# Optimization experiments

Measured on AMD Instinct MI355X. Metric: run time of the kernel, lower is better.

## Reference

```python
import jax, jax.numpy as jnp
import numpy as np

L, B, D, H, FFN, V = 6, 16, 1024, 16, 4096, 32000
CACHE, SRC, MAXPOS = 512, 512, 1024
HD = D // H
SCALING = HD ** -0.5


def _sinusoidal_pe():
    # MarianMT format: first half sin, second half cos (not interleaved)
    half = D // 2
    emb = np.exp(np.arange(half, dtype=np.float32) * (-np.log(10000.0) / (half - 1)))
    pos = np.arange(MAXPOS, dtype=np.float32)[:, None]
    pe = np.concatenate([np.sin(pos * emb), np.cos(pos * emb)], axis=1)
    return jnp.asarray(pe, jnp.float32)


def setup_inputs() -> dict:
    key = jax.random.key(0)
    keys = iter(jax.random.split(key, 64))
    def rn(shape, s=0.02):
        return jax.random.normal(next(keys), shape, jnp.float32) * s
    inp = {
        'decoder_embed': rn((B, 1, D), 1.0),
        'encoder_hidden_states': rn((B, SRC, D), 1.0),
        'past_keys': rn((L, B, CACHE, D), 1.0),
        'past_values': rn((L, B, CACHE, D), 1.0),
        'cache_len': jnp.array([256], jnp.int32),
        'pe': _sinusoidal_pe(),
    }
    for name in ['sa_qw', 'sa_kw', 'sa_vw', 'sa_ow', 'ca_qw', 'ca_kw', 'ca_vw', 'ca_ow']:
        inp[name] = rn((L, D, D))
    for name in ['sa_qb', 'sa_kb', 'sa_vb', 'sa_ob', 'ca_qb', 'ca_kb', 'ca_vb', 'ca_ob']:
        inp[name] = rn((L, D))
    inp['fc1_w'] = rn((L, FFN, D)); inp['fc1_b'] = rn((L, FFN))
    inp['fc2_w'] = rn((L, D, FFN)); inp['fc2_b'] = rn((L, D))
    for name in ['ln1_w', 'ln2_w', 'ln3_w']:
        inp[name] = jnp.ones((L, D), jnp.float32)
    for name in ['ln1_b', 'ln2_b', 'ln3_b']:
        inp[name] = jnp.zeros((L, D), jnp.float32)
    inp['lm_w'] = rn((V, D))
    return inp


def _lin(x, w, b):
    # torch nn.Linear: w is [out, in]
    return jnp.einsum('...i,oi->...o', x, w) + b


def _ln(x, w, b):
    m = jnp.mean(x, -1, keepdims=True)
    v = jnp.var(x, -1, keepdims=True)
    return (x - m) * jax.lax.rsqrt(v + 1e-5) * w + b


def _heads(x):
    # [B, S, D] -> [B, H, S, HD]
    b, s, _ = x.shape
    return x.reshape(b, s, H, HD).transpose(0, 2, 1, 3)


def _attend(q, k, v, bias):
    w = jnp.einsum('bhqd,bhkd->bhqk', q * SCALING, k)
    if bias is not None:
        w = w + bias
    a = jax.nn.softmax(w, axis=-1)
    o = jnp.einsum('bhqk,bhkd->bhqd', a, v)
    b = o.shape[0]
    return o.transpose(0, 2, 1, 3).reshape(b, -1, D)


def reference(decoder_embed, encoder_hidden_states, past_keys, past_values, cache_len, pe,
              sa_qw, sa_kw, sa_vw, sa_ow, ca_qw, ca_kw, ca_vw, ca_ow,
              sa_qb, sa_kb, sa_vb, sa_ob, ca_qb, ca_kb, ca_vb, ca_ob,
              fc1_w, fc1_b, fc2_w, fc2_b,
              ln1_w, ln1_b, ln2_w, ln2_b, ln3_w, ln3_b, lm_w):
    embed_scale = jnp.asarray(np.sqrt(float(D)), jnp.float32)
    pos = jax.lax.dynamic_slice_in_dim(pe, cache_len[0], 1, axis=0)[None]  # [1,1,D]
    h = decoder_embed * embed_scale + pos
    # Faithful to original: cache_len tensor is passed as attn_mask and
    # broadcast-added to attention logits (a constant shift, no-op post-softmax).
    mask_bias = cache_len.astype(h.dtype)
    new_ks, new_vs = [], []
    for i in range(L):
        # self-attention with KV cache concat
        res = h
        q = _lin(h, sa_qw[i], sa_qb[i])
        nk = _lin(h, sa_kw[i], sa_kb[i])
        nv = _lin(h, sa_vw[i], sa_vb[i])
        fk = jnp.concatenate([past_keys[i], nk], axis=1)   # [B, CACHE+1, D]
        fv = jnp.concatenate([past_values[i], nv], axis=1)
        attn = _attend(_heads(q), _heads(fk), _heads(fv), mask_bias)
        h = _ln(res + _lin(attn, sa_ow[i], sa_ob[i]), ln1_w[i], ln1_b[i])
        # cross-attention (no mask)
        res = h
        q = _lin(h, ca_qw[i], ca_qb[i])
        ek = _lin(encoder_hidden_states, ca_kw[i], ca_kb[i])
        ev = _lin(encoder_hidden_states, ca_vw[i], ca_vb[i])
        attn = _attend(_heads(q), _heads(ek), _heads(ev), None)
        h = _ln(res + _lin(attn, ca_ow[i], ca_ob[i]), ln2_w[i], ln2_b[i])
        # FFN with SiLU
        res = h
        ff = _lin(jax.nn.silu(_lin(h, fc1_w[i], fc1_b[i])), fc2_w[i], fc2_b[i])
        h = _ln(res + ff, ln3_w[i], ln3_b[i])
        new_ks.append(nk)
        new_vs.append(nv)
    logits = jnp.einsum('bsd,vd->bsv', h, lm_w)  # lm_head, no bias
    return (logits, jnp.stack(new_ks, 0), jnp.stack(new_vs, 0))
```

## Files before the change

kernel.cpp:

```cpp
#include <hip/hip_runtime.h>
#include <math.h>

#define LYRS 6
#define BATCH 16
#define DIM 1024
#define NH 16
#define HDIM 64
#define FFNDIM 4096
#define VOCAB 32000
#define NCACHE 512
#define SRCLEN 512
#define SCALE 0.125f
#define EMB_SCALE 32.0f
#define BD (BATCH * DIM)
#define BF (BATCH * FFNDIM)
#define BV (BATCH * VOCAB)

__device__ __forceinline__ float wave_reduce_sum(float v){
#pragma unroll
  for (int off = 32; off; off >>= 1) v += __shfl_xor(v, off, 64);
  return v;
}
__device__ __forceinline__ float wave_reduce_max(float v){
#pragma unroll
  for (int off = 32; off; off >>= 1) v = fmaxf(v, __shfl_xor(v, off, 64));
  return v;
}
__device__ __forceinline__ float4 silu4(float4 v){
  v.x = v.x / (1.f + __expf(-v.x));
  v.y = v.y / (1.f + __expf(-v.y));
  v.z = v.z / (1.f + __expf(-v.z));
  v.w = v.w / (1.f + __expf(-v.w));
  return v;
}

__global__ __launch_bounds__(256) void k_embed(const float* __restrict__ de,
                                               const float* __restrict__ pe,
                                               const int* __restrict__ cl,
                                               float* __restrict__ h){
  int b = blockIdx.x, t = threadIdx.x;
  int c = cl[0];
  const float4* d4 = (const float4*)(de + (size_t)b * DIM);
  const float4* p4 = (const float4*)(pe + (size_t)c * DIM);
  float4* h4 = (float4*)(h + (size_t)b * DIM);
  float4 a = d4[t], p = p4[t];
  float4 o;
  o.x = a.x * EMB_SCALE + p.x; o.y = a.y * EMB_SCALE + p.y;
  o.z = a.z * EMB_SCALE + p.z; o.w = a.w * EMB_SCALE + p.w;
  h4[t] = o;
}

template<int KPB, int NZ, bool SILU>
__device__ __forceinline__ void gemv_ms_core(
    const float* __restrict__ Asrc, int a_rs, int pz,
    const float* __restrict__ abias,
    const float* __restrict__ W, int w_rs,
    float* __restrict__ Cz, int c_rs,
    int n0, int k0){
  __shared__ float As[16][KPB];
  const int tid = threadIdx.x;
  {
    const int m = tid >> 4;
    const int q0 = (tid & 15) * 4;
    constexpr int QPT = KPB / 64;
#pragma unroll
    for (int qq = 0; qq < QPT; ++qq){
      const int q = q0 + qq * 64;
      const int gk = k0 + q;
      float4 v;
      if (NZ == 0){
        v = *(const float4*)(Asrc + (size_t)m * a_rs + gk);
      } else {
        if (abias) v = *(const float4*)(abias + gk);
        else { v.x = 0.f; v.y = 0.f; v.z = 0.f; v.w = 0.f; }
#pragma unroll
        for (int z = 0; z < NZ; ++z){
          float4 pv = *(const float4*)(Asrc + (size_t)z * pz + (size_t)m * a_rs + gk);
          v.x += pv.x; v.y += pv.y; v.z += pv.z; v.w += pv.w;
        }
      }
      if (SILU) v = silu4(v);
      *(float4*)(&As[m][q]) = v;
    }
  }
  __syncthreads();
  const int lane = tid & 63;
  const int m0 = (tid >> 6) * 4;
  const float* Wrow = W + (size_t)(n0 + lane) * w_rs + k0;
  float acc0 = 0.f, acc1 = 0.f, acc2 = 0.f, acc3 = 0.f;
  constexpr int CHUNKS = KPB / 64;
  float4 wb[2][16];
#pragma unroll
  for (int c = 0; c < 16; ++c) wb[0][c] = *(const float4*)(Wrow + c * 4);
#pragma unroll
  for (int ch = 0; ch < CHUNKS; ++ch){
    const int cur = ch & 1;
    if (ch + 1 < CHUNKS){
#pragma unroll
      for (int c = 0; c < 16; ++c)
        wb[cur ^ 1][c] = *(const float4*)(Wrow + (ch + 1) * 64 + c * 4);
    }
#pragma unroll
    for (int c = 0; c < 16; ++c){
      float4 wv = wb[cur][c];
      const int q = ch * 64 + c * 4;
      float4 a0 = *(const float4*)(&As[m0 + 0][q]);
      float4 a1 = *(const float4*)(&As[m0 + 1][q]);
      float4 a2 = *(const float4*)(&As[m0 + 2][q]);
      float4 a3 = *(const float4*)(&As[m0 + 3][q]);
      acc0 = fmaf(wv.x, a0.x, acc0); acc0 = fmaf(wv.y, a0.y, acc0);
      acc0 = fmaf(wv.z, a0.z, acc0); acc0 = fmaf(wv.w, a0.w, acc0);
      acc1 = fmaf(wv.x, a1.x, acc1); acc1 = fmaf(wv.y, a1.y, acc1);
      acc1 = fmaf(wv.z, a1.z, acc1); acc1 = fmaf(wv.w, a1.w, acc1);
      acc2 = fmaf(wv.x, a2.x, acc2); acc2 = fmaf(wv.y, a2.y, acc2);
      acc2 = fmaf(wv.z, a2.z, acc2); acc2 = fmaf(wv.w, a2.w, acc2);
      acc3 = fmaf(wv.x, a3.x, acc3); acc3 = fmaf(wv.y, a3.y, acc3);
      acc3 = fmaf(wv.z, a3.z, acc3); acc3 = fmaf(wv.w, a3.w, acc3);
    }
  }
  Cz[(size_t)(m0 + 0) * c_rs + n0 + lane] = acc0;
  Cz[(size_t)(m0 + 1) * c_rs + n0 + lane] = acc1;
  Cz[(size_t)(m0 + 2) * c_rs + n0 + lane] = acc2;
  Cz[(size_t)(m0 + 3) * c_rs + n0 + lane] = acc3;
}

template<int KPB, int NZ, bool SILU>
__global__ __launch_bounds__(256) void k_gemv_ms(
    const float* __restrict__ A, int a_rs, int a_bs, int pz,
    const float* __restrict__ abias,
    const float* __restrict__ W, int w_rs, int w_bs,
    float* __restrict__ C, int c_rs, int c_bs, int c_zs){
  const int bb = blockIdx.y;
  gemv_ms_core<KPB, NZ, SILU>(A + (size_t)bb * a_bs, a_rs, pz, abias,
      W + (size_t)bb * w_bs, w_rs,
      C + (size_t)blockIdx.z * c_zs + (size_t)bb * c_bs, c_rs,
      blockIdx.x * 64, blockIdx.z * KPB);
}

template<int KPB>
__global__ __launch_bounds__(256) void k_gemv_ms3(
    const float* __restrict__ A, const float* __restrict__ W0,
    const float* __restrict__ W1, const float* __restrict__ W2,
    float* __restrict__ C){
  const int y = blockIdx.y;
  const float* W = (y == 0) ? W0 : ((y == 1) ? W1 : W2);
  gemv_ms_core<KPB, 0, false>(A, DIM, 0, nullptr, W, DIM,
      C + ((size_t)y * 4 + blockIdx.z) * BD, DIM,
      blockIdx.x * 64, blockIdx.z * KPB);
}

__global__ __launch_bounds__(256) void k_fin2(const float* __restrict__ P,
                                              float* __restrict__ out){
  int i = blockIdx.x * 256 + threadIdx.x;
  out[i] = P[i] + P[(size_t)BV + i];
}

__global__ __launch_bounds__(512) void k_self_attn(
    const float* __restrict__ Pqkv, const float* __restrict__ qb_,
    const float* __restrict__ kb_, const float* __restrict__ vb_,
    const float* __restrict__ pk, const float* __restrict__ pv,
    float* __restrict__ satt, float* __restrict__ out_k,
    float* __restrict__ out_v){
  __shared__ float qs[64], ks[64], vs[64];
  __shared__ float sc[513];
  __shared__ float red1[8], red2[8];
  __shared__ float o8[8][64];
  const int bh = blockIdx.x, b = bh >> 4, h = bh & 15;
  const int tid = threadIdx.x, w = tid >> 6, lane = tid & 63;
  const int hd = h * HDIM + lane;
  if (w < 3){
    const float* Pz = Pqkv + (size_t)w * (4 * BD);
    const float* bias = (w == 0) ? qb_ : ((w == 1) ? kb_ : vb_);
    float v = bias[hd];
#pragma unroll
    for (int z = 0; z < 4; ++z)
      v += Pz[(size_t)z * BD + b * DIM + hd];
    if (w == 0) qs[lane] = v * SCALE;
    else if (w == 1){ ks[lane] = v; out_k[b * DIM + hd] = v; }
    else { vs[lane] = v; out_v[b * DIM + hd] = v; }
  }
  __syncthreads();
  const int jj = lane >> 4, c = lane & 15;
  float4 q4 = *(const float4*)(&qs[c * 4]);
  const float* kbase = pk + (size_t)b * NCACHE * DIM + h * HDIM + c * 4;
  {
    float4 nk = *(const float4*)(kbase + (size_t)(w * 4 + jj) * DIM);
    for (int it = 0; it < 16; ++it){
      int j = it * 32 + w * 4 + jj;
      float4 K4 = nk;
      if (it < 15) nk = *(const float4*)(kbase + (size_t)(j + 32) * DIM);
      float r = q4.x * K4.x;
      r = fmaf(q4.y, K4.y, r); r = fmaf(q4.z, K4.z, r); r = fmaf(q4.w, K4.w, r);
      r += __shfl_xor(r, 1, 64); r += __shfl_xor(r, 2, 64);
      r += __shfl_xor(r, 4, 64); r += __shfl_xor(r, 8, 64);
      if (c == 0) sc[j] = r;
    }
  }
  if (w == 0 && lane < 16){
    float4 k4 = *(const float4*)(&ks[lane * 4]);
    float r = q4.x * k4.x;
    r = fmaf(q4.y, k4.y, r); r = fmaf(q4.z, k4.z, r); r = fmaf(q4.w, k4.w, r);
    r += __shfl_xor(r, 1, 64); r += __shfl_xor(r, 2, 64);
// ... 26 lines not shown
  float4 acc; acc.x = 0.f; acc.y = 0.f; acc.z = 0.f; acc.w = 0.f;
  {
    float4 nv = *(const float4*)(vbase + (size_t)(w * 4 + jj) * DIM);
    for (int it = 0; it < 16; ++it){
      int j = it * 32 + w * 4 + jj;
      float4 V4 = nv;
      if (it < 15) nv = *(const float4*)(vbase + (size_t)(j + 32) * DIM);
      float pj = sc[j];
      acc.x = fmaf(pj, V4.x, acc.x); acc.y = fmaf(pj, V4.y, acc.y);
      acc.z = fmaf(pj, V4.z, acc.z); acc.w = fmaf(pj, V4.w, acc.w);
    }
  }
  if (w == 0 && lane < 16){
    float p512 = sc[512];
    float4 v4 = *(const float4*)(&vs[lane * 4]);
    acc.x = fmaf(p512, v4.x, acc.x); acc.y = fmaf(p512, v4.y, acc.y);
    acc.z = fmaf(p512, v4.z, acc.z); acc.w = fmaf(p512, v4.w, acc.w);
  }
  acc.x += __shfl_xor(acc.x, 16, 64); acc.x += __shfl_xor(acc.x, 32, 64);
  acc.y += __shfl_xor(acc.y, 16, 64); acc.y += __shfl_xor(acc.y, 32, 64);
  acc.z += __shfl_xor(acc.z, 16, 64); acc.z += __shfl_xor(acc.z, 32, 64);
  acc.w += __shfl_xor(acc.w, 16, 64); acc.w += __shfl_xor(acc.w, 32, 64);
  if (lane < 16){
    o8[w][lane * 4 + 0] = acc.x; o8[w][lane * 4 + 1] = acc.y;
    o8[w][lane * 4 + 2] = acc.z; o8[w][lane * 4 + 3] = acc.w;
  }
  __syncthreads();
  if (tid < 64){
    float s2 = 0.f;
#pragma unroll
    for (int ww = 0; ww < 8; ++ww) s2 += o8[ww][tid];
    satt[b * DIM + h * HDIM + tid] = s2 * inv;
  }
}

template<int NZ>
__global__ __launch_bounds__(256) void k_add_ln_pz(
    const float* __restrict__ res, const float* __restrict__ P, int zs,
    const float* __restrict__ obias, const float* __restrict__ w,
    const float* __restrict__ bln, float* __restrict__ outh){
  __shared__ float r1[4], r2[4];
  int b = blockIdx.x, tid = threadIdx.x, wave = tid >> 6, lane = tid & 63;
  float4 rv = ((const float4*)(res + (size_t)b * DIM))[tid];
  float4 ob = ((const float4*)obias)[tid];
  float v0 = rv.x + ob.x, v1 = rv.y + ob.y, v2 = rv.z + ob.z, v3 = rv.w + ob.w;
#pragma unroll
  for (int z = 0; z < NZ; ++z){
    float4 pz = ((const float4*)(P + (size_t)z * zs + (size_t)b * DIM))[tid];
    v0 += pz.x; v1 += pz.y; v2 += pz.z; v3 += pz.w;
  }
  float s = v0 + v1 + v2 + v3;
  float sq = v0 * v0 + v1 * v1 + v2 * v2 + v3 * v3;
  s = wave_reduce_sum(s); sq = wave_reduce_sum(sq);
  if (lane == 0){ r1[wave] = s; r2[wave] = sq; }
  __syncthreads();
  float ts = r1[0] + r1[1] + r1[2] + r1[3];
  float tq = r2[0] + r2[1] + r2[2] + r2[3];
  float mean = ts * (1.f / DIM);
  float var = tq * (1.f / DIM) - mean * mean;
  float rstd = rsqrtf(var + 1e-5f);
  float4 wv = ((const float4*)w)[tid], bv = ((const float4*)bln)[tid];
  float4 o;
  o.x = (v0 - mean) * rstd * wv.x + bv.x;
  o.y = (v1 - mean) * rstd * wv.y + bv.y;
  o.z = (v2 - mean) * rstd * wv.z + bv.z;
  o.w = (v3 - mean) * rstd * wv.w + bv.w;
  ((float4*)(outh + (size_t)b * DIM))[tid] = o;
}

__global__ __launch_bounds__(256) void k_gmat2(
    const float* __restrict__ Pcq, const float* __restrict__ caqb,
    const float* __restrict__ kw, float* __restrict__ g){
  __shared__ float qsT[64][16];
  __shared__ float Ps[4][16][64];
  const int h = blockIdx.y, c0 = blockIdx.x * 64;
  const int tid = threadIdx.x, lane = tid & 63, wave = tid >> 6;
  {
    const int b = tid >> 4, q0 = (tid & 15) * 4;
    float4 v = *(const float4*)(caqb + h * HDIM + q0);
#pragma unroll
    for (int z = 0; z < 8; ++z){
      float4 pv = *(const float4*)(Pcq + (size_t)z * BD +
                                   (size_t)b * DIM + h * HDIM + q0);
      v.x += pv.x; v.y += pv.y; v.z += pv.z; v.w += pv.w;
    }
    qsT[q0 + 0][b] = v.x * SCALE; qsT[q0 + 1][b] = v.y * SCALE;
    qsT[q0 + 2][b] = v.z * SCALE; qsT[q0 + 3][b] = v.w * SCALE;
  }
  __syncthreads();
  float wv[16];
#pragma unroll
  for (int dd = 0; dd < 16; ++dd)
    wv[dd] = kw[(size_t)(h * HDIM + wave * 16 + dd) * DIM + c0 + lane];
  float acc[16];
#pragma unroll
  for (int m = 0; m < 16; ++m) acc[m] = 0.f;
#pragma unroll
  for (int dd = 0; dd < 16; ++dd){
    const int d = wave * 16 + dd;
    float4 a0 = *(const float4*)(&qsT[d][0]);
// ... 119 lines not shown
  const float* pv   = (const float*)d_in[3];
  const int*   cl   = (const int*)d_in[4];
  const float* pe   = (const float*)d_in[5];
  const float* saqw = (const float*)d_in[6];
  const float* sakw = (const float*)d_in[7];
  const float* savw = (const float*)d_in[8];
  const float* saow = (const float*)d_in[9];
  const float* caqw = (const float*)d_in[10];
  const float* cakw = (const float*)d_in[11];
  const float* cavw = (const float*)d_in[12];
  const float* caow = (const float*)d_in[13];
  const float* saqb = (const float*)d_in[14];
  const float* sakb = (const float*)d_in[15];
  const float* savb = (const float*)d_in[16];
  const float* saob = (const float*)d_in[17];
  const float* caqb = (const float*)d_in[18];
  const float* cakb = (const float*)d_in[19];
  const float* cavb = (const float*)d_in[20];
  const float* caob = (const float*)d_in[21];
  const float* fc1w = (const float*)d_in[22];
  const float* fc1b = (const float*)d_in[23];
  const float* fc2w = (const float*)d_in[24];
  const float* fc2b = (const float*)d_in[25];
  const float* ln1w = (const float*)d_in[26];
  const float* ln2w = (const float*)d_in[27];
  const float* ln3w = (const float*)d_in[28];
  const float* ln1b = (const float*)d_in[29];
  const float* ln2b = (const float*)d_in[30];
  const float* ln3b = (const float*)d_in[31];
  const float* lmw  = (const float*)d_in[32];
  float* out = (float*)d_out;
  float* ws  = (float*)d_ws;

  float* h    = ws;
  float* satt = ws + 16384;
  float* g    = ws + 32768;
  float* ctx  = ws + 294912;
  float* Pqkv = ws + 557056;
  float* Po   = ws + 950272;
  float* Pcq  = ws + 1212416;
  float* Pvo  = ws + 1474560;
  float* Pco  = ws + 1736704;
  float* Pf1  = ws + 1998848;
  float* Pf2  = ws + 2523136;
  float* s2b  = ws + 3047424;
  float* Plm  = ws + 4096000;

  float* out_k = out + 512000;
  float* out_v = out + 610304;

  k_embed<<<16, 256, 0, stream>>>(de, pe, cl, h);

  for (int i = 0; i < LYRS; ++i){
    size_t wo = (size_t)i * DIM * DIM;
    size_t bo = (size_t)i * DIM;
    float* ko = out_k + (size_t)i * BD;
    float* vo = out_v + (size_t)i * BD;
    k_gemv_ms3<256><<<dim3(16, 3, 4), 256, 0, stream>>>(h, saqw + wo, sakw + wo,
        savw + wo, Pqkv);
    k_self_attn<<<256, 512, 0, stream>>>(Pqkv, saqb + bo, sakb + bo, savb + bo,
        pk + (size_t)i * BATCH * NCACHE * DIM, pv + (size_t)i * BATCH * NCACHE * DIM,
        satt, ko, vo);
    k_gemv_ms<128, 0, false><<<dim3(16, 1, 8), 256, 0, stream>>>(satt, DIM, 0, 0,
        nullptr, saow + wo, DIM, 0, Po, DIM, 0, BD);
    k_add_ln_pz<8><<<16, 256, 0, stream>>>(h, Po, BD, saob + bo,
        ln1w + bo, ln1b + bo, h);
    k_gemv_ms<128, 0, false><<<dim3(16, 1, 8), 256, 0, stream>>>(h, DIM, 0, 0,
        nullptr, caqw + wo, DIM, 0, Pcq, DIM, 0, BD);
    k_gmat2<<<dim3(16, 16), 256, 0, stream>>>(Pcq, caqb + bo, cakw + wo, g);
    k_gemv_ms<512, 0, false><<<dim3(8, 16, 2), 256, 0, stream>>>(g, DIM, NH * DIM,
        0, nullptr, enc, DIM, SRCLEN * DIM, s2b, SRCLEN, NH * SRCLEN,
        BATCH * NH * SRCLEN);
    k_ctx_sm<<<dim3(16, 16), 256, 0, stream>>>(s2b, enc, ctx);
    k_gemv_ms<128, 0, false><<<dim3(1, 16, 8), 256, 0, stream>>>(ctx, NH * DIM,
        DIM, 0, nullptr, cavw + wo, DIM, HDIM * DIM, Pvo, DIM, HDIM, BD);
    k_gemv_ms<128, 8, false><<<dim3(16, 1, 8), 256, 0, stream>>>(Pvo, DIM, 0,
        BD, cavb + bo, caow + wo, DIM, 0, Pco, DIM, 0, BD);
    k_add_ln_pz<8><<<16, 256, 0, stream>>>(h, Pco, BD, caob + bo,
        ln2w + bo, ln2b + bo, h);
    k_gemv_ms<256, 0, false><<<dim3(64, 1, 4), 256, 0, stream>>>(h, DIM, 0, 0,
        nullptr, fc1w + (size_t)i * FFNDIM * DIM, DIM, 0, Pf1, FFNDIM, 0, BF);
    k_gemv_ms<128, 4, true><<<dim3(16, 1, 32), 256, 0, stream>>>(Pf1, FFNDIM, 0,
        BF, fc1b + (size_t)i * FFNDIM,
        fc2w + (size_t)i * DIM * FFNDIM, FFNDIM, 0, Pf2, DIM, 0, BD);
    k_add_ln_pz<32><<<16, 256, 0, stream>>>(h, Pf2, BD, fc2b + bo,
        ln3w + bo, ln3b + bo, h);
  }
  k_gemv_ms<512, 0, false><<<dim3(VOCAB / 64, 1, 2), 256, 0, stream>>>(h, DIM, 0,
      0, nullptr, lmw, DIM, 0, Plm, VOCAB, 0, BV);
  k_fin2<<<BV / 256, 256, 0, stream>>>(Plm, out);
}
```

Baseline: 847.1 us.

## Fuse residual-add LayerNorm into following GEMV prologues and use atomic split-K

```diff
diff --git a/kernel.cpp b/kernel.cpp
--- a/kernel.cpp
+++ b/kernel.cpp
@@ -51,40 +51,85 @@
 }
 
 template<int KPB, int NZ, bool SILU>
-__device__ __forceinline__ void gemv_ms_core(
+__device__ __forceinline__ void plain_stage(float (*As)[KPB],
     const float* __restrict__ Asrc, int a_rs, int pz,
-    const float* __restrict__ abias,
-    const float* __restrict__ W, int w_rs,
-    float* __restrict__ Cz, int c_rs,
-    int n0, int k0){
-  __shared__ float As[16][KPB];
+    const float* __restrict__ abias, int k0){
   const int tid = threadIdx.x;
-  {
-    const int m = tid >> 4;
-    const int q0 = (tid & 15) * 4;
-    constexpr int QPT = KPB / 64;
-#pragma unroll
-    for (int qq = 0; qq < QPT; ++qq){
-      const int q = q0 + qq * 64;
-      const int gk = k0 + q;
-      float4 v;
-      if (NZ == 0){
-        v = *(const float4*)(Asrc + (size_t)m * a_rs + gk);
-      } else {
-        if (abias) v = *(const float4*)(abias + gk);
-        else { v.x = 0.f; v.y = 0.f; v.z = 0.f; v.w = 0.f; }
-#pragma unroll
-        for (int z = 0; z < NZ; ++z){
-          float4 pv = *(const float4*)(Asrc + (size_t)z * pz + (size_t)m * a_rs + gk);
-          v.x += pv.x; v.y += pv.y; v.z += pv.z; v.w += pv.w;
-        }
+  const int m = tid >> 4, q0 = (tid & 15) * 4;
+#pragma unroll
+  for (int qq = 0; qq < KPB / 64; ++qq){
+    const int q = q0 + qq * 64;
+    const int gk = k0 + q;
+    float4 v;
+    if (NZ == 0){
+      v = *(const float4*)(Asrc + (size_t)m * a_rs + gk);
+    } else {
+      if (abias) v = *(const float4*)(abias + gk);
+      else { v.x = 0.f; v.y = 0.f; v.z = 0.f; v.w = 0.f; }
+#pragma unroll
+      for (int z = 0; z < NZ; ++z){
+        float4 pv = *(const float4*)(Asrc + (size_t)z * pz + (size_t)m * a_rs + gk);
+        v.x += pv.x; v.y += pv.y; v.z += pv.z; v.w += pv.w;
       }
-      if (SILU) v = silu4(v);
-      *(float4*)(&As[m][q]) = v;
-    }
-  }
-  __syncthreads();
-  const int lane = tid & 63;
+    }
+    if (SILU) v = silu4(v);
+    *(float4*)(&As[m][q]) = v;
+  }
+  __syncthreads();
+}
+
+template<int KPB>
+__device__ __forceinline__ void ln_stage(float (*As)[KPB],
+    const float* __restrict__ res, const float* __restrict__ acc,
+    const float* __restrict__ obias, const float* __restrict__ lnw,
+    const float* __restrict__ lnb, int k0, float* __restrict__ hout){
+  const int tid = threadIdx.x;
+  const int m = tid >> 4, t = tid & 15;
+  const float* rr = res + (size_t)m * DIM;
+  const float* ar = acc + (size_t)m * DIM;
+  float s = 0.f, sq = 0.f;
+#pragma unroll
+  for (int c = 0; c < 16; ++c){
+    const int k = t * 4 + c * 64;
+    float4 rv = *(const float4*)(rr + k);
+    float4 av = *(const float4*)(ar + k);
+    float4 ob = *(const float4*)(obias + k);
+    float x0 = rv.x + av.x + ob.x, x1 = rv.y + av.y + ob.y;
+    float x2 = rv.z + av.z + ob.z, x3 = rv.w + av.w + ob.w;
+    s += x0 + x1 + x2 + x3;
+    sq += x0 * x0 + x1 * x1 + x2 * x2 + x3 * x3;
+  }
+#pragma unroll
+  for (int o = 1; o <= 8; o <<= 1){
+    s += __shfl_xor(s, o, 64); sq += __shfl_xor(sq, o, 64);
+  }
+  const float mean = s * (1.f / DIM);
+  const float rstd = rsqrtf(sq * (1.f / DIM) - mean * mean + 1e-5f);
+#pragma unroll
+  for (int qq = 0; qq < KPB / 64; ++qq){
+    const int q = t * 4 + qq * 64;
+    const int k = k0 + q;
+    float4 rv = *(const float4*)(rr + k);
+    float4 av = *(const float4*)(ar + k);
+    float4 ob = *(const float4*)(obias + k);
+    float4 wv = *(const float4*)(lnw + k);
+    float4 bv = *(const float4*)(lnb + k);
+    float4 o4;
+    o4.x = (rv.x + av.x + ob.x - mean) * rstd * wv.x + bv.x;
+    o4.y = (rv.y + av.y + ob.y - mean) * rstd * wv.y + bv.y;
+    o4.z = (rv.z + av.z + ob.z - mean) * rstd * wv.z + bv.z;
+    o4.w = (rv.w + av.w + ob.w - mean) * rstd * wv.w + bv.w;
+    *(float4*)(&As[m][q]) = o4;
+    if (hout) *(float4*)(hout + (size_t)m * DIM + k) = o4;
+  }
+  __syncthreads();
+}
+
+template<int KPB, bool ATOMIC>
+__device__ __forceinline__ void gemv_w_loop(float (*As)[KPB],
+    const float* __restrict__ W, int w_rs, float* __restrict__ Cz,
+    int c_rs, int n0, int k0){
+  const int tid = threadIdx.x, lane = tid & 63;
   const int m0 = (tid >> 6) * 4;
   const float* Wrow = W + (size_t)(n0 + lane) * w_rs + k0;
   float acc0 = 0.f, acc1 = 0.f, acc2 = 0.f, acc3 = 0.f;
@@ -118,21 +163,30 @@
       acc3 = fmaf(wv.z, a3.z, acc3); acc3 = fmaf(wv.w, a3.w, acc3);
     }
   }
-  Cz[(size_t)(m0 + 0) * c_rs + n0 + lane] = acc0;
-  Cz[(size_t)(m0 + 1) * c_rs + n0 + lane] = acc1;
-  Cz[(size_t)(m0 + 2) * c_rs + n0 + lane] = acc2;
-  Cz[(size_t)(m0 + 3) * c_rs + n0 + lane] = acc3;
-}
-
-template<int KPB, int NZ, bool SILU>
+  if (ATOMIC){
+    atomicAdd(&Cz[(size_t)(m0 + 0) * c_rs + n0 + lane], acc0);
+    atomicAdd(&Cz[(size_t)(m0 + 1) * c_rs + n0 + lane], acc1);
+    atomicAdd(&Cz[(size_t)(m0 + 2) * c_rs + n0 + lane], acc2);
+    atomicAdd(&Cz[(size_t)(m0 + 3) * c_rs + n0 + lane], acc3);
+  } else {
+    Cz[(size_t)(m0 + 0) * c_rs + n0 + lane] = acc0;
+    Cz[(size_t)(m0 + 1) * c_rs + n0 + lane] = acc1;
+    Cz[(size_t)(m0 + 2) * c_rs + n0 + lane] = acc2;
+    Cz[(size_t)(m0 + 3) * c_rs + n0 + lane] = acc3;
+  }
+}
+
+template<int KPB, int NZ, bool SILU, bool ATOMIC>
 __global__ __launch_bounds__(256) void k_gemv_ms(
     const float* __restrict__ A, int a_rs, int a_bs, int pz,
     const float* __restrict__ abias,
     const float* __restrict__ W, int w_rs, int w_bs,
     float* __restrict__ C, int c_rs, int c_bs, int c_zs){
+  __shared__ float As[16][KPB];
   const int bb = blockIdx.y;
-  gemv_ms_core<KPB, NZ, SILU>(A + (size_t)bb * a_bs, a_rs, pz, abias,
-      W + (size_t)bb * w_bs, w_rs,
+  plain_stage<KPB, NZ, SILU>(As, A + (size_t)bb * a_bs, a_rs, pz, abias,
+                             blockIdx.z * KPB);
+  gemv_w_loop<KPB, ATOMIC>(As, W + (size_t)bb * w_bs, w_rs,
       C + (size_t)blockIdx.z * c_zs + (size_t)bb * c_bs, c_rs,
       blockIdx.x * 64, blockIdx.z * KPB);
 }
@@ -142,9 +196,42 @@
     const float* __restrict__ A, const float* __restrict__ W0,
     const float* __restrict__ W1, const float* __restrict__ W2,
     float* __restrict__ C){
+  __shared__ float As[16][KPB];
   const int y = blockIdx.y;
   const float* W = (y == 0) ? W0 : ((y == 1) ? W1 : W2);
-  gemv_ms_core<KPB, 0, false>(A, DIM, 0, nullptr, W, DIM,
+  plain_stage<KPB, 0, false>(As, A, DIM, 0, nullptr, blockIdx.z * KPB);
+  gemv_w_loop<KPB, false>(As, W, DIM,
+      C + ((size_t)y * 4 + blockIdx.z) * BD, DIM,
+      blockIdx.x * 64, blockIdx.z * KPB);
+}
+
+template<int KPB>
+__global__ __launch_bounds__(256) void k_gemv_ln(
+    const float* __restrict__ res, const float* __restrict__ acc,
+    const float* __restrict__ obias, const float* __restrict__ lnw,
+    const float* __restrict__ lnb, const float* __restrict__ W,
+    float* __restrict__ hout, float* __restrict__ C, int c_rs, int c_zs){
+  __shared__ float As[16][KPB];
+  float* hw = (blockIdx.x == 0) ? hout : nullptr;
+  ln_stage<KPB>(As, res, acc, obias, lnw, lnb, blockIdx.z * KPB, hw);
+  gemv_w_loop<KPB, false>(As, W, DIM, C + (size_t)blockIdx.z * c_zs, c_rs,
+      blockIdx.x * 64, blockIdx.z * KPB);
+}
+
+template<int KPB>
+__global__ __launch_bounds__(256) void k_gemv_ln3(
+    const float* __restrict__ res, const float* __restrict__ acc,
+    const float* __restrict__ obias, const float* __restrict__ lnw,
+    const float* __restrict__ lnb,
+    const float* __restrict__ W0, const float* __restrict__ W1,
+    const float* __restrict__ W2,
+    float* __restrict__ hout, float* __restrict__ C){
+  __shared__ float As[16][KPB];
+  const int y = blockIdx.y;
+  const float* W = (y == 0) ? W0 : ((y == 1) ? W1 : W2);
+  float* hw = (blockIdx.x == 0 && y == 0) ? hout : nullptr;
+  ln_stage<KPB>(As, res, acc, obias, lnw, lnb, blockIdx.z * KPB, hw);
+  gemv_w_loop<KPB, false>(As, W, DIM,
       C + ((size_t)y * 4 + blockIdx.z) * BD, DIM,
       blockIdx.x * 64, blockIdx.z * KPB);
 }
@@ -160,7 +247,7 @@
     const float* __restrict__ kb_, const float* __restrict__ vb_,
     const float* __restrict__ pk, const float* __restrict__ pv,
     float* __restrict__ satt, float* __restrict__ out_k,
-    float* __restrict__ out_v){
+    float* __restrict__ out_v, float* __restrict__ azero){
   __shared__ float qs[64], ks[64], vs[64];
   __shared__ float sc[513];
   __shared__ float red1[8], red2[8];
@@ -168,6 +255,10 @@
   const int bh = blockIdx.x, b = bh >> 4, h = bh & 15;
   const int tid = threadIdx.x, w = tid >> 6, lane = tid & 63;
   const int hd = h * HDIM + lane;
+  if (tid < 48){
+    float4 z4; z4.x = 0.f; z4.y = 0.f; z4.z = 0.f; z4.w = 0.f;
+    ((float4*)azero)[(size_t)bh * 48 + tid] = z4;
+  }
   if (w < 3){
     const float* Pz = Pqkv + (size_t)w * (4 * BD);
     const float* bias = (w == 0) ? qb_ : ((w == 1) ? kb_ : vb_);
@@ -260,40 +351,6 @@
     for (int ww = 0; ww < 8; ++ww) s2 += o8[ww][tid];
     satt[b * DIM + h * HDIM + tid] = s2 * inv;
   }
-}
-
-template<int NZ>
-__global__ __launch_bounds__(256) void k_add_ln_pz(
-    const float* __restrict__ res, const float* __restrict__ P, int zs,
-    const float* __restrict__ obias, const float* __restrict__ w,
-    const float* __restrict__ bln, float* __restrict__ outh){
-  __shared__ float r1[4], r2[4];
-  int b = blockIdx.x, tid = threadIdx.x, wave = tid >> 6, lane = tid & 63;
-  float4 rv = ((const float4*)(res + (size_t)b * DIM))[tid];
-  float4 ob = ((const float4*)obias)[tid];
-  float v0 = rv.x + ob.x, v1 = rv.y + ob.y, v2 = rv.z + ob.z, v3 = rv.w + ob.w;
-#pragma unroll
-  for (int z = 0; z < NZ; ++z){
-    float4 pz = ((const float4*)(P + (size_t)z * zs + (size_t)b * DIM))[tid];
-    v0 += pz.x; v1 += pz.y; v2 += pz.z; v3 += pz.w;
-  }
-  float s = v0 + v1 + v2 + v3;
-  float sq = v0 * v0 + v1 * v1 + v2 * v2 + v3 * v3;
-  s = wave_reduce_sum(s); sq = wave_reduce_sum(sq);
-  if (lane == 0){ r1[wave] = s; r2[wave] = sq; }
-  __syncthreads();
-  float ts = r1[0] + r1[1] + r1[2] + r1[3];
-  float tq = r2[0] + r2[1] + r2[2] + r2[3];
-  float mean = ts * (1.f / DIM);
-  float var = tq * (1.f / DIM) - mean * mean;
-  float rstd = rsqrtf(var + 1e-5f);
-  float4 wv = ((const float4*)w)[tid], bv = ((const float4*)bln)[tid];
-  float4 o;
-  o.x = (v0 - mean) * rstd * wv.x + bv.x;
-  o.y = (v1 - mean) * rstd * wv.y + bv.y;
-  o.z = (v2 - mean) * rstd * wv.z + bv.z;
-  o.w = (v3 - mean) * rstd * wv.w + bv.w;
-  ((float4*)(outh + (size_t)b * DIM))[tid] = o;
 }
 
 __global__ __launch_bounds__(256) void k_gmat2(
@@ -479,61 +536,70 @@
   float* out = (float*)d_out;
   float* ws  = (float*)d_ws;
 
-  float* h    = ws;
-  float* satt = ws + 16384;
-  float* g    = ws + 32768;
-  float* ctx  = ws + 294912;
-  float* Pqkv = ws + 557056;
-  float* Po   = ws + 950272;
-  float* Pcq  = ws + 1212416;
-  float* Pvo  = ws + 1474560;
-  float* Pco  = ws + 1736704;
-  float* Pf1  = ws + 1998848;
-  float* Pf2  = ws + 2523136;
-  float* s2b  = ws + 3047424;
-  float* Plm  = ws + 4096000;
+  float* h3buf = ws;
+  float* h1buf = ws + 16384;
+  float* h2buf = ws + 32768;
+  float* satt  = ws + 49152;
+  float* Abuf  = ws + 65536;
+  float* A_o   = Abuf;
+  float* A_co  = Abuf + 16384;
+  float* A_f2  = Abuf + 32768;
+  float* g     = ws + 114688;
+  float* ctx   = ws + 376832;
+  float* Pqkv  = ws + 638976;
+  float* Pcq   = ws + 835584;
+  float* Pvo   = ws + 966656;
+  float* Pf1   = ws + 1097728;
+  float* s2b   = ws + 1359872;
+  float* Plm   = ws + 1622016;
 
   float* out_k = out + 512000;
   float* out_v = out + 610304;
 
-  k_embed<<<16, 256, 0, stream>>>(de, pe, cl, h);
+  k_embed<<<16, 256, 0, stream>>>(de, pe, cl, h3buf);
 
   for (int i = 0; i < LYRS; ++i){
     size_t wo = (size_t)i * DIM * DIM;
     size_t bo = (size_t)i * DIM;
     float* ko = out_k + (size_t)i * BD;
     float* vo = out_v + (size_t)i * BD;
-    k_gemv_ms3<256><<<dim3(16, 3, 4), 256, 0, stream>>>(h, saqw + wo, sakw + wo,
-        savw + wo, Pqkv);
+    const float* pk_l = pk + (size_t)i * BATCH * NCACHE * DIM;
+    const float* pv_l = pv + (size_t)i * BATCH * NCACHE * DIM;
+    if (i == 0){
+      k_gemv_ms3<256><<<dim3(16, 3, 4), 256, 0, stream>>>(h3buf,
+          saqw + wo, sakw + wo, savw + wo, Pqkv);
+    } else {
+      size_t po = (size_t)(i - 1) * DIM;
+      k_gemv_ln3<256><<<dim3(16, 3, 4), 256, 0, stream>>>(h2buf, A_f2,
+          fc2b + po, ln3w + po, ln3b + po,
+          saqw + wo, sakw + wo, savw + wo, h3buf, Pqkv);
+    }
     k_self_attn<<<256, 512, 0, stream>>>(Pqkv, saqb + bo, sakb + bo, savb + bo,
-        pk + (size_t)i * BATCH * NCACHE * DIM, pv + (size_t)i * BATCH * NCACHE * DIM,
-        satt, ko, vo);
-    k_gemv_ms<128, 0, false><<<dim3(16, 1, 8), 256, 0, stream>>>(satt, DIM, 0, 0,
-        nullptr, saow + wo, DIM, 0, Po, DIM, 0, BD);
-    k_add_ln_pz<8><<<16, 256, 0, stream>>>(h, Po, BD, saob + bo,
-        ln1w + bo, ln1b + bo, h);
-    k_gemv_ms<128, 0, false><<<dim3(16, 1, 8), 256, 0, stream>>>(h, DIM, 0, 0,
-        nullptr, caqw + wo, DIM, 0, Pcq, DIM, 0, BD);
+        pk_l, pv_l, satt, ko, vo, Abuf);
+    k_gemv_ms<128, 0, false, true><<<dim3(16, 1, 8), 256, 0, stream>>>(satt,
+        DIM, 0, 0, nullptr, saow + wo, DIM, 0, A_o, DIM, 0, 0);
+    k_gemv_ln<128><<<dim3(16, 1, 8), 256, 0, stream>>>(h3buf, A_o, saob + bo,
+        ln1w + bo, ln1b + bo, caqw + wo, h1buf, Pcq, DIM, BD);
     k_gmat2<<<dim3(16, 16), 256, 0, stream>>>(Pcq, caqb + bo, cakw + wo, g);
-    k_gemv_ms<512, 0, false><<<dim3(8, 16, 2), 256, 0, stream>>>(g, DIM, NH * DIM,
-        0, nullptr, enc, DIM, SRCLEN * DIM, s2b, SRCLEN, NH * SRCLEN,
+    k_gemv_ms<512, 0, false, false><<<dim3(8, 16, 2), 256, 0, stream>>>(g, DIM,
+        NH * DIM, 0, nullptr, enc, DIM, SRCLEN * DIM, s2b, SRCLEN, NH * SRCLEN,
         BATCH * NH * SRCLEN);
     k_ctx_sm<<<dim3(16, 16), 256, 0, stream>>>(s2b, enc, ctx);
-    k_gemv_ms<128, 0, false><<<dim3(1, 16, 8), 256, 0, stream>>>(ctx, NH * DIM,
-        DIM, 0, nullptr, cavw + wo, DIM, HDIM * DIM, Pvo, DIM, HDIM, BD);
-    k_gemv_ms<128, 8, false><<<dim3(16, 1, 8), 256, 0, stream>>>(Pvo, DIM, 0,
-        BD, cavb + bo, caow + wo, DIM, 0, Pco, DIM, 0, BD);
-    k_add_ln_pz<8><<<16, 256, 0, stream>>>(h, Pco, BD, caob + bo,
-        ln2w + bo, ln2b + bo, h);
-    k_gemv_ms<256, 0, false><<<dim3(64, 1, 4), 256, 0, stream>>>(h, DIM, 0, 0,
-        nullptr, fc1w + (size_t)i * FFNDIM * DIM, DIM, 0, Pf1, FFNDIM, 0, BF);
-    k_gemv_ms<128, 4, true><<<dim3(16, 1, 32), 256, 0, stream>>>(Pf1, FFNDIM, 0,
-        BF, fc1b + (size_t)i * FFNDIM,
-        fc2w + (size_t)i * DIM * FFNDIM, FFNDIM, 0, Pf2, DIM, 0, BD);
-    k_add_ln_pz<32><<<16, 256, 0, stream>>>(h, Pf2, BD, fc2b + bo,
-        ln3w + bo, ln3b + bo, h);
-  }
-  k_gemv_ms<512, 0, false><<<dim3(VOCAB / 64, 1, 2), 256, 0, stream>>>(h, DIM, 0,
-      0, nullptr, lmw, DIM, 0, Plm, VOCAB, 0, BV);
+    k_gemv_ms<128, 0, false, false><<<dim3(1, 16, 8), 256, 0, stream>>>(ctx,
+        NH * DIM, DIM, 0, nullptr, cavw + wo, DIM, HDIM * DIM, Pvo, DIM, HDIM, BD);
+    k_gemv_ms<128, 8, false, true><<<dim3(16, 1, 8), 256, 0, stream>>>(Pvo,
+        DIM, 0, BD, cavb + bo, caow + wo, DIM, 0, A_co, DIM, 0, 0);
+    k_gemv_ln<256><<<dim3(64, 1, 4), 256, 0, stream>>>(h1buf, A_co, caob + bo,
+        ln2w + bo, ln2b + bo, fc1w + (size_t)i * FFNDIM * DIM, h2buf,
+        Pf1, FFNDIM, BF);
+    k_gemv_ms<256, 4, true, true><<<dim3(16, 1, 16), 256, 0, stream>>>(Pf1,
+        FFNDIM, 0, BF, fc1b + (size_t)i * FFNDIM,
+        fc2w + (size_t)i * DIM * FFNDIM, FFNDIM, 0, A_f2, DIM, 0, 0);
+  }
+  {
+    size_t po = (size_t)(LYRS - 1) * DIM;
+    k_gemv_ln<512><<<dim3(500, 1, 2), 256, 0, stream>>>(h2buf, A_f2,
+        fc2b + po, ln3w + po, ln3b + po, lmw, nullptr, Plm, VOCAB, BV);
+  }
   k_fin2<<<BV / 256, 256, 0, stream>>>(Plm, out);
 }
```

Result: slower. 890.7 us (+5.2%).

## Fuse residual LayerNorm into following GEMV via inter-block flag sync

Applied to the files above, without the earlier changes.

```diff
diff --git a/kernel.cpp b/kernel.cpp
--- a/kernel.cpp
+++ b/kernel.cpp
@@ -34,57 +34,60 @@
   return v;
 }
 
-__global__ __launch_bounds__(256) void k_embed(const float* __restrict__ de,
-                                               const float* __restrict__ pe,
-                                               const int* __restrict__ cl,
-                                               float* __restrict__ h){
-  int b = blockIdx.x, t = threadIdx.x;
-  int c = cl[0];
-  const float4* d4 = (const float4*)(de + (size_t)b * DIM);
-  const float4* p4 = (const float4*)(pe + (size_t)c * DIM);
-  float4* h4 = (float4*)(h + (size_t)b * DIM);
-  float4 a = d4[t], p = p4[t];
-  float4 o;
-  o.x = a.x * EMB_SCALE + p.x; o.y = a.y * EMB_SCALE + p.y;
-  o.z = a.z * EMB_SCALE + p.z; o.w = a.w * EMB_SCALE + p.w;
-  h4[t] = o;
+__device__ __forceinline__ float4 gld4(const float* p){
+  unsigned long long a = __hip_atomic_load((const unsigned long long*)p,
+      __ATOMIC_RELAXED, __HIP_MEMORY_SCOPE_AGENT);
+  unsigned long long b = __hip_atomic_load((const unsigned long long*)(p + 2),
+      __ATOMIC_RELAXED, __HIP_MEMORY_SCOPE_AGENT);
+  float4 r;
+  r.x = __uint_as_float((unsigned)a); r.y = __uint_as_float((unsigned)(a >> 32));
+  r.z = __uint_as_float((unsigned)b); r.w = __uint_as_float((unsigned)(b >> 32));
+  return r;
+}
+__device__ __forceinline__ void gst4(float* p, float4 v){
+  unsigned long long a = (unsigned long long)__float_as_uint(v.x) |
+                         ((unsigned long long)__float_as_uint(v.y) << 32);
+  unsigned long long b = (unsigned long long)__float_as_uint(v.z) |
+                         ((unsigned long long)__float_as_uint(v.w) << 32);
+  __hip_atomic_store((unsigned long long*)p, a, __ATOMIC_RELAXED,
+                     __HIP_MEMORY_SCOPE_AGENT);
+  __hip_atomic_store((unsigned long long*)(p + 2), b, __ATOMIC_RELAXED,
+                     __HIP_MEMORY_SCOPE_AGENT);
 }
 
 template<int KPB, int NZ, bool SILU>
-__device__ __forceinline__ void gemv_ms_core(
+__device__ __forceinline__ void plain_stage(float (*As)[KPB],
     const float* __restrict__ Asrc, int a_rs, int pz,
-    const float* __restrict__ abias,
-    const float* __restrict__ W, int w_rs,
-    float* __restrict__ Cz, int c_rs,
-    int n0, int k0){
-  __shared__ float As[16][KPB];
+    const float* __restrict__ abias, int k0){
   const int tid = threadIdx.x;
-  {
-    const int m = tid >> 4;
-    const int q0 = (tid & 15) * 4;
-    constexpr int QPT = KPB / 64;
-#pragma unroll
-    for (int qq = 0; qq < QPT; ++qq){
-      const int q = q0 + qq * 64;
-      const int gk = k0 + q;
-      float4 v;
-      if (NZ == 0){
-        v = *(const float4*)(Asrc + (size_t)m * a_rs + gk);
-      } else {
-        if (abias) v = *(const float4*)(abias + gk);
-        else { v.x = 0.f; v.y = 0.f; v.z = 0.f; v.w = 0.f; }
-#pragma unroll
-        for (int z = 0; z < NZ; ++z){
-          float4 pv = *(const float4*)(Asrc + (size_t)z * pz + (size_t)m * a_rs + gk);
-          v.x += pv.x; v.y += pv.y; v.z += pv.z; v.w += pv.w;
-        }
+  const int m = tid >> 4, q0 = (tid & 15) * 4;
+#pragma unroll
+  for (int qq = 0; qq < KPB / 64; ++qq){
+    const int q = q0 + qq * 64;
+    const int gk = k0 + q;
+    float4 v;
+    if (NZ == 0){
+      v = *(const float4*)(Asrc + (size_t)m * a_rs + gk);
+    } else {
+      if (abias) v = *(const float4*)(abias + gk);
+      else { v.x = 0.f; v.y = 0.f; v.z = 0.f; v.w = 0.f; }
+#pragma unroll
+      for (int z = 0; z < NZ; ++z){
+        float4 pv = *(const float4*)(Asrc + (size_t)z * pz + (size_t)m * a_rs + gk);
+        v.x += pv.x; v.y += pv.y; v.z += pv.z; v.w += pv.w;
       }
-      if (SILU) v = silu4(v);
-      *(float4*)(&As[m][q]) = v;
-    }
-  }
-  __syncthreads();
-  const int lane = tid & 63;
+    }
+    if (SILU) v = silu4(v);
+    *(float4*)(&As[m][q]) = v;
+  }
+  __syncthreads();
+}
+
+template<int KPB>
+__device__ __forceinline__ void gemv_w_loop(float (*As)[KPB],
+    const float* __restrict__ W, int w_rs, float* __restrict__ Cz,
+    int c_rs, int n0, int k0){
+  const int tid = threadIdx.x, lane = tid & 63;
   const int m0 = (tid >> 6) * 4;
   const float* Wrow = W + (size_t)(n0 + lane) * w_rs + k0;
   float acc0 = 0.f, acc1 = 0.f, acc2 = 0.f, acc3 = 0.f;
@@ -130,29 +133,159 @@
     const float* __restrict__ abias,
     const float* __restrict__ W, int w_rs, int w_bs,
     float* __restrict__ C, int c_rs, int c_bs, int c_zs){
+  __shared__ float As[16][KPB];
   const int bb = blockIdx.y;
-  gemv_ms_core<KPB, NZ, SILU>(A + (size_t)bb * a_bs, a_rs, pz, abias,
-      W + (size_t)bb * w_bs, w_rs,
+  plain_stage<KPB, NZ, SILU>(As, A + (size_t)bb * a_bs, a_rs, pz, abias,
+                             blockIdx.z * KPB);
+  gemv_w_loop<KPB>(As, W + (size_t)bb * w_bs, w_rs,
       C + (size_t)blockIdx.z * c_zs + (size_t)bb * c_bs, c_rs,
       blockIdx.x * 64, blockIdx.z * KPB);
 }
 
-template<int KPB>
-__global__ __launch_bounds__(256) void k_gemv_ms3(
-    const float* __restrict__ A, const float* __restrict__ W0,
-    const float* __restrict__ W1, const float* __restrict__ W2,
-    float* __restrict__ C){
-  const int y = blockIdx.y;
-  const float* W = (y == 0) ? W0 : ((y == 1) ? W1 : W2);
-  gemv_ms_core<KPB, 0, false>(A, DIM, 0, nullptr, W, DIM,
-      C + ((size_t)y * 4 + blockIdx.z) * BD, DIM,
-      blockIdx.x * 64, blockIdx.z * KPB);
-}
-
-__global__ __launch_bounds__(256) void k_fin2(const float* __restrict__ P,
-                                              float* __restrict__ out){
-  int i = blockIdx.x * 256 + threadIdx.x;
-  out[i] = P[i] + P[(size_t)BV + i];
+__global__ __launch_bounds__(256) void k_qkv0(
+    const float* __restrict__ de, const float* __restrict__ pe,
+    const int* __restrict__ cl,
+    const float* __restrict__ W0, const float* __restrict__ W1,
+    const float* __restrict__ W2,
+    float* __restrict__ hout, float* __restrict__ C){
+  __shared__ float As[16][256];
+  const int bx = blockIdx.x, by = blockIdx.y, bz = blockIdx.z;
+  const int tid = threadIdx.x;
+  const int k0 = bz * 256;
+  const int c = cl[0];
+  {
+    const int m = tid >> 4, q0 = (tid & 15) * 4;
+#pragma unroll
+    for (int qq = 0; qq < 4; ++qq){
+      const int q = q0 + qq * 64, gk = k0 + q;
+      float4 a = *(const float4*)(de + (size_t)m * DIM + gk);
+      float4 p = *(const float4*)(pe + (size_t)c * DIM + gk);
+      float4 v;
+      v.x = a.x * EMB_SCALE + p.x; v.y = a.y * EMB_SCALE + p.y;
+      v.z = a.z * EMB_SCALE + p.z; v.w = a.w * EMB_SCALE + p.w;
+      *(float4*)(&As[m][q]) = v;
+      if (bx == 0 && by == 0)
+        *(float4*)(hout + (size_t)m * DIM + gk) = v;
+    }
+  }
+  __syncthreads();
+  const float* W = (by == 0) ? W0 : ((by == 1) ? W1 : W2);
+  gemv_w_loop<256>(As, W, DIM, C + (size_t)(by * 4 + bz) * BD, DIM,
+                   bx * 64, k0);
+}
+
+template<int NZ>
+__device__ void ln_row(int b, const float* __restrict__ res,
+    const float* __restrict__ P, int pzs, const float* __restrict__ obias,
+    const float* __restrict__ lnw, const float* __restrict__ lnb,
+    float* __restrict__ hout, int* __restrict__ flags, int gen){
+  __shared__ float r1[4], r2[4];
+  const int tid = threadIdx.x, wave = tid >> 6, lane = tid & 63;
+  float4 x = ((const float4*)(res + (size_t)b * DIM))[tid];
+  float4 ob = ((const float4*)obias)[tid];
+  x.x += ob.x; x.y += ob.y; x.z += ob.z; x.w += ob.w;
+#pragma unroll
+  for (int z = 0; z < NZ; ++z){
+    float4 p = ((const float4*)(P + (size_t)z * pzs + (size_t)b * DIM))[tid];
+    x.x += p.x; x.y += p.y; x.z += p.z; x.w += p.w;
+  }
+  float s = x.x + x.y + x.z + x.w;
+  float sq = x.x * x.x + x.y * x.y + x.z * x.z + x.w * x.w;
+  s = wave_reduce_sum(s); sq = wave_reduce_sum(sq);
+  if (lane == 0){ r1[wave] = s; r2[wave] = sq; }
+  __syncthreads();
+  float ts = r1[0] + r1[1] + r1[2] + r1[3];
+  float tq = r2[0] + r2[1] + r2[2] + r2[3];
+  float mean = ts * (1.f / DIM);
+  float rstd = rsqrtf(tq * (1.f / DIM) - mean * mean + 1e-5f);
+  float4 wv = ((const float4*)lnw)[tid], bv = ((const float4*)lnb)[tid];
+  float4 o;
+  o.x = (x.x - mean) * rstd * wv.x + bv.x;
+  o.y = (x.y - mean) * rstd * wv.y + bv.y;
+  o.z = (x.z - mean) * rstd * wv.z + bv.z;
+  o.w = (x.w - mean) * rstd * wv.w + bv.w;
+  gst4(hout + (size_t)b * DIM + tid * 4, o);
+  __syncthreads();
+  if (tid == 0)
+    __hip_atomic_store(&flags[b * 32], gen, __ATOMIC_RELEASE,
+                       __HIP_MEMORY_SCOPE_AGENT);
+}
+
+__device__ __forceinline__ void flag_wait16(const int* __restrict__ flags,
+                                            int gen){
+  if (threadIdx.x < 16){
+    while (__hip_atomic_load(&flags[threadIdx.x * 32], __ATOMIC_ACQUIRE,
+                             __HIP_MEMORY_SCOPE_AGENT) < gen)
+      __builtin_amdgcn_s_sleep(2);
+  }
+  __syncthreads();
+}
+
+template<int KPB, int NZ>
+__global__ __launch_bounds__(256) void k_gemv_lnf(
+    const float* __restrict__ res, const float* __restrict__ P, int pzs,
+    const float* __restrict__ obias, const float* __restrict__ lnw,
+    const float* __restrict__ lnb,
+    const float* __restrict__ W0, const float* __restrict__ W1,
+    const float* __restrict__ W2,
+    float* __restrict__ hout, int* __restrict__ flags, int gen,
+    float* __restrict__ C, int c_rs, int slab_elems){
+  __shared__ float As[16][KPB];
+  const int bx = blockIdx.x, by = blockIdx.y, bz = blockIdx.z;
+  const int tid = threadIdx.x, lane = tid & 63;
+  const int k0 = bz * KPB, n0 = bx * 64;
+  const float* W = (by == 0) ? W0 : ((by == 1) ? W1 : W2);
+  const float* Wrow = W + (size_t)(n0 + lane) * DIM + k0;
+  constexpr int CHUNKS = KPB / 64;
+  float4 wb[2][16];
+#pragma unroll
+  for (int c = 0; c < 16; ++c) wb[0][c] = *(const float4*)(Wrow + c * 4);
+  if (by == 0 && bz == 0 && bx < 16)
+    ln_row<NZ>(bx, res, P, pzs, obias, lnw, lnb, hout, flags, gen);
+  flag_wait16(flags, gen);
+  {
+    const int m = tid >> 4, q0 = (tid & 15) * 4;
+#pragma unroll
+    for (int qq = 0; qq < KPB / 64; ++qq){
+      const int q = q0 + qq * 64;
+      float4 v = gld4(hout + (size_t)m * DIM + k0 + q);
+      *(float4*)(&As[m][q]) = v;
+    }
+  }
+  __syncthreads();
+  const int m0 = (tid >> 6) * 4;
+  float acc0 = 0.f, acc1 = 0.f, acc2 = 0.f, acc3 = 0.f;
+#pragma unroll
+  for (int ch = 0; ch < CHUNKS; ++ch){
+    const int cur = ch & 1;
+    if (ch + 1 < CHUNKS){
+#pragma unroll
+      for (int c = 0; c < 16; ++c)
+        wb[cur ^ 1][c] = *(const float4*)(Wrow + (ch + 1) * 64 + c * 4);
+    }
+#pragma unroll
+    for (int c = 0; c < 16; ++c){
+      float4 wv = wb[cur][c];
+      const int q = ch * 64 + c * 4;
+      float4 a0 = *(const float4*)(&As[m0 + 0][q]);
+      float4 a1 = *(const float4*)(&As[m0 + 1][q]);
+      float4 a2 = *(const float4*)(&As[m0 + 2][q]);
+      float4 a3 = *(const float4*)(&As[m0 + 3][q]);
+      acc0 = fmaf(wv.x, a0.x, acc0); acc0 = fmaf(wv.y, a0.y, acc0);
+      acc0 = fmaf(wv.z, a0.z, acc0); acc0 = fmaf(wv.w, a0.w, acc0);
+      acc1 = fmaf(wv.x, a1.x, acc1); acc1 = fmaf(wv.y, a1.y, acc1);
+      acc1 = fmaf(wv.z, a1.z, acc1); acc1 = fmaf(wv.w, a1.w, acc1);
+      acc2 = fmaf(wv.x, a2.x, acc2); acc2 = fmaf(wv.y, a2.y, acc2);
+      acc2 = fmaf(wv.z, a2.z, acc2); acc2 = fmaf(wv.w, a2.w, acc2);
+      acc3 = fmaf(wv.x, a3.x, acc3); acc3 = fmaf(wv.y, a3.y, acc3);
+      acc3 = fmaf(wv.z, a3.z, acc3); acc3 = fmaf(wv.w, a3.w, acc3);
+    }
+  }
+  float* Cz = C + (size_t)(by * gridDim.z + bz) * slab_elems;
+  Cz[(size_t)(m0 + 0) * c_rs + n0 + lane] = acc0;
+  Cz[(size_t)(m0 + 1) * c_rs + n0 + lane] = acc1;
+  Cz[(size_t)(m0 + 2) * c_rs + n0 + lane] = acc2;
+  Cz[(size_t)(m0 + 3) * c_rs + n0 + lane] = acc3;
 }
 
 __global__ __launch_bounds__(512) void k_self_attn(
@@ -479,61 +612,73 @@
   float* out = (float*)d_out;
   float* ws  = (float*)d_ws;
 
-  float* h    = ws;
-  float* satt = ws + 16384;
-  float* g    = ws + 32768;
-  float* ctx  = ws + 294912;
-  float* Pqkv = ws + 557056;
-  float* Po   = ws + 950272;
-  float* Pcq  = ws + 1212416;
-  float* Pvo  = ws + 1474560;
-  float* Pco  = ws + 1736704;
-  float* Pf1  = ws + 1998848;
-  float* Pf2  = ws + 2523136;
-  float* s2b  = ws + 3047424;
-  float* Plm  = ws + 4096000;
+  int* flags   = (int*)ws;
+  float* h3buf = ws + 1024;
+  float* h1buf = h3buf + 16384;
+  float* h2buf = h1buf + 16384;
+  float* satt  = h2buf + 16384;
+  float* g     = satt + 16384;
+  float* ctx   = g + 262144;
+  float* Pqkv  = ctx + 262144;
+  float* Po    = Pqkv + 196608;
+  float* Pcq   = Po + 131072;
+  float* Pvo   = Pcq + 131072;
+  float* Pco   = Pvo + 131072;
+  float* Pf1   = Pco + 131072;
+  float* Pf2   = Pf1 + 262144;
+  float* s2b   = Pf2 + 524288;
 
   float* out_k = out + 512000;
   float* out_v = out + 610304;
 
-  k_embed<<<16, 256, 0, stream>>>(de, pe, cl, h);
+  hipMemsetAsync(d_ws, 0, 2048, stream);
+  int gen = 0;
 
   for (int i = 0; i < LYRS; ++i){
     size_t wo = (size_t)i * DIM * DIM;
     size_t bo = (size_t)i * DIM;
     float* ko = out_k + (size_t)i * BD;
     float* vo = out_v + (size_t)i * BD;
-    k_gemv_ms3<256><<<dim3(16, 3, 4), 256, 0, stream>>>(h, saqw + wo, sakw + wo,
-        savw + wo, Pqkv);
+    const float* pk_l = pk + (size_t)i * BATCH * NCACHE * DIM;
+    const float* pv_l = pv + (size_t)i * BATCH * NCACHE * DIM;
+    if (i == 0){
+      k_qkv0<<<dim3(16, 3, 4), 256, 0, stream>>>(de, pe, cl,
+          saqw + wo, sakw + wo, savw + wo, h3buf, Pqkv);
+    } else {
+      size_t po = (size_t)(i - 1) * DIM;
+      k_gemv_lnf<256, 32><<<dim3(16, 3, 4), 256, 0, stream>>>(h2buf, Pf2, BD,
+          fc2b + po, ln3w + po, ln3b + po,
+          saqw + wo, sakw + wo, savw + wo, h3buf, flags, ++gen, Pqkv, DIM, BD);
+    }
     k_self_attn<<<256, 512, 0, stream>>>(Pqkv, saqb + bo, sakb + bo, savb + bo,
-        pk + (size_t)i * BATCH * NCACHE * DIM, pv + (size_t)i * BATCH * NCACHE * DIM,
-        satt, ko, vo);
-    k_gemv_ms<128, 0, false><<<dim3(16, 1, 8), 256, 0, stream>>>(satt, DIM, 0, 0,
-        nullptr, saow + wo, DIM, 0, Po, DIM, 0, BD);
-    k_add_ln_pz<8><<<16, 256, 0, stream>>>(h, Po, BD, saob + bo,
-        ln1w + bo, ln1b + bo, h);
-    k_gemv_ms<128, 0, false><<<dim3(16, 1, 8), 256, 0, stream>>>(h, DIM, 0, 0,
-        nullptr, caqw + wo, DIM, 0, Pcq, DIM, 0, BD);
+        pk_l, pv_l, satt, ko, vo);
+    k_gemv_ms<128, 0, false><<<dim3(16, 1, 8), 256, 0, stream>>>(satt, DIM, 0,
+        0, nullptr, saow + wo, DIM, 0, Po, DIM, 0, BD);
+    k_gemv_lnf<128, 8><<<dim3(16, 1, 8), 256, 0, stream>>>(h3buf, Po, BD,
+        saob + bo, ln1w + bo, ln1b + bo,
+        caqw + wo, nullptr, nullptr, h1buf, flags, ++gen, Pcq, DIM, BD);
     k_gmat2<<<dim3(16, 16), 256, 0, stream>>>(Pcq, caqb + bo, cakw + wo, g);
-    k_gemv_ms<512, 0, false><<<dim3(8, 16, 2), 256, 0, stream>>>(g, DIM, NH * DIM,
-        0, nullptr, enc, DIM, SRCLEN * DIM, s2b, SRCLEN, NH * SRCLEN,
+    k_gemv_ms<512, 0, false><<<dim3(8, 16, 2), 256, 0, stream>>>(g, DIM,
+        NH * DIM, 0, nullptr, enc, DIM, SRCLEN * DIM, s2b, SRCLEN, NH * SRCLEN,
         BATCH * NH * SRCLEN);
     k_ctx_sm<<<dim3(16, 16), 256, 0, stream>>>(s2b, enc, ctx);
-    k_gemv_ms<128, 0, false><<<dim3(1, 16, 8), 256, 0, stream>>>(ctx, NH * DIM,
-        DIM, 0, nullptr, cavw + wo, DIM, HDIM * DIM, Pvo, DIM, HDIM, BD);
+    k_gemv_ms<128, 0, false><<<dim3(1, 16, 8), 256, 0, stream>>>(ctx,
+        NH * DIM, DIM, 0, nullptr, cavw + wo, DIM, HDIM * DIM, Pvo, DIM, HDIM, BD);
     k_gemv_ms<128, 8, false><<<dim3(16, 1, 8), 256, 0, stream>>>(Pvo, DIM, 0,
         BD, cavb + bo, caow + wo, DIM, 0, Pco, DIM, 0, BD);
-    k_add_ln_pz<8><<<16, 256, 0, stream>>>(h, Pco, BD, caob + bo,
-        ln2w + bo, ln2b + bo, h);
-    k_gemv_ms<256, 0, false><<<dim3(64, 1, 4), 256, 0, stream>>>(h, DIM, 0, 0,
-        nullptr, fc1w + (size_t)i * FFNDIM * DIM, DIM, 0, Pf1, FFNDIM, 0, BF);
+    k_gemv_lnf<256, 8><<<dim3(64, 1, 4), 256, 0, stream>>>(h1buf, Pco, BD,
+        caob + bo, ln2w + bo, ln2b + bo,
+        fc1w + (size_t)i * FFNDIM * DIM, nullptr, nullptr,
+        h2buf, flags, ++gen, Pf1, FFNDIM, BF);
     k_gemv_ms<128, 4, true><<<dim3(16, 1, 32), 256, 0, stream>>>(Pf1, FFNDIM, 0,
         BF, fc1b + (size_t)i * FFNDIM,
         fc2w + (size_t)i * DIM * FFNDIM, FFNDIM, 0, Pf2, DIM, 0, BD);
-    k_add_ln_pz<32><<<16, 256, 0, stream>>>(h, Pf2, BD, fc2b + bo,
-        ln3w + bo, ln3b + bo, h);
-  }
-  k_gemv_ms<512, 0, false><<<dim3(VOCAB / 64, 1, 2), 256, 0, stream>>>(h, DIM, 0,
-      0, nullptr, lmw, DIM, 0, Plm, VOCAB, 0, BV);
-  k_fin2<<<BV / 256, 256, 0, stream>>>(Plm, out);
-}
+  }
+  {
+    size_t po = (size_t)(LYRS - 1) * DIM;
+    k_add_ln_pz<32><<<16, 256, 0, stream>>>(h2buf, Pf2, BD, fc2b + po,
+        ln3w + po, ln3b + po, h3buf);
+  }
+  k_gemv_ms<1024, 0, false><<<dim3(VOCAB / 64, 1, 1), 256, 0, stream>>>(h3buf,
+      DIM, 0, 0, nullptr, lmw, DIM, 0, out, VOCAB, 0, 0);
+}
```

New measurement: 1.156 ms. 1.36x slower.
